# Kernel optimization log

Hardware: AMD Instinct MI355X
Metric: run time of the kernel (lower is better)

The kernel has to match this reference:

```python
import jax, jax.numpy as jnp
import numpy as np

N, F_IN, F_OUT, K = 4096, 32, 32, 2
NEG_SLOPE = 0.2
MASK_VAL = -9e15


def _sparse_mat(kv, km, density=0.01):
    vals = jax.random.normal(kv, (N, N), dtype=jnp.float32)
    mask = jax.random.uniform(km, (N, N)) < density
    return vals * mask


def setup_inputs() -> dict:
    key = jax.random.key(0)
    ks = jax.random.split(key, 12)
    x = jax.random.normal(ks[0], (N, F_IN), dtype=jnp.float32)
    Ld = _sparse_mat(ks[1], ks[2])
    Lu = _sparse_mat(ks[3], ks[4])
    P = jax.random.normal(ks[5], (N, N), dtype=jnp.float32) / np.sqrt(N)
    W1 = jax.random.normal(ks[6], (K, F_IN, F_OUT), dtype=jnp.float32) * 0.1
    W2 = jax.random.normal(ks[7], (K, F_IN, F_OUT), dtype=jnp.float32) * 0.1
    W0 = jax.random.normal(ks[8], (F_IN, F_OUT), dtype=jnp.float32) * 0.1
    att1 = jax.random.normal(ks[9], (2 * F_OUT * K, 1), dtype=jnp.float32) * 0.1
    att2 = jax.random.normal(ks[10], (2 * F_OUT * K, 1), dtype=jnp.float32) * 0.1
    return {"x": x, "Ld": Ld, "Lu": Lu, "P": P, "W1": W1, "W2": W2,
            "W0": W0, "att1": att1, "att2": att2}


def _branch(x, L, W, att):
    # W: [K, F_in, F_out]; precompute x @ W[k] for all k -> [K, N, F_out]
    Kk, _, Fo = W.shape
    xw = jnp.einsum('nf,kfo->kno', x, W)
    # torch.cat([x@W[k]], dim=1) == transpose+reshape of xw
    xcat = jnp.transpose(xw, (1, 0, 2)).reshape(x.shape[0], Kk * Fo)
    d = Fo * Kk
    e = xcat @ att[:d] + (xcat @ att[d:]).T            # [N, N]
    e = jax.nn.leaky_relu(e, negative_slope=NEG_SLOPE)
    e = jnp.where(L != 0, e, MASK_VAL)
    alpha = jax.nn.softmax(e, axis=1)                   # row softmax, no dropout (eval)
    z = alpha @ xw[0]
    a = alpha
    for k in range(1, Kk):
        a = a @ L
        z = z + a @ xw[k]
    return z


def reference(x, Ld, Lu, P, W1, W2, W0, att1, att2):
    z1 = _branch(x, Ld, W1, att1)
    z2 = _branch(x, Lu, W2, att2)
    x0 = P @ (x @ W0)
    return z1 + z2 + x0
```

## Files before the change

kernel.cpp:

```cpp
#include <hip/hip_runtime.h>
#include <hip/hip_bf16.h>

#define NN 4096
#define CAP 128
#define KS 8

typedef __attribute__((ext_vector_type(8))) short bf16x8;
typedef __attribute__((ext_vector_type(4))) float f32x4;

__device__ __forceinline__ float lrelu(float v) { return v >= 0.f ? v : 0.2f * v; }

__device__ __forceinline__ ushort f2bu(float f) {
    unsigned u = __float_as_uint(f);
    return (ushort)((u + 0x7FFFu + ((u >> 16) & 1u)) >> 16);
}

__global__ __launch_bounds__(256) void k_prep(
    const float* __restrict__ x,
    const float* __restrict__ W1, const float* __restrict__ W2,
    const float* __restrict__ W0,
    const float* __restrict__ att1, const float* __restrict__ att2,
    float* __restrict__ xwA1, float* __restrict__ xwB1,
    float* __restrict__ xwA2, float* __restrict__ xwB2,
    float* __restrict__ a1, float* __restrict__ b1,
    float* __restrict__ a2, float* __restrict__ b2,
    __hip_bfloat16* __restrict__ Bt)
{
    __shared__ float wl[5120];
    __shared__ float xs[256];
    const int t = threadIdx.x;
    for (int i = t; i < 2048; i += 256) { wl[i] = W1[i]; wl[2048 + i] = W2[i]; }
    for (int i = t; i < 1024; i += 256) wl[4096 + i] = W0[i];
    const int rowBase = blockIdx.x * 8;
    xs[t] = x[rowBase * 32 + t];
    __syncthreads();

    const int o = t & 31, r = t >> 5;
    const int row = rowBase + r;
    const float* xr = &xs[r * 32];
    float vA1 = 0.f, vB1 = 0.f, vA2 = 0.f, vB2 = 0.f, v0 = 0.f;
#pragma unroll
    for (int f = 0; f < 32; ++f) {
        const float xv = xr[f];
        vA1 += xv * wl[f * 32 + o];
        vB1 += xv * wl[1024 + f * 32 + o];
        vA2 += xv * wl[2048 + f * 32 + o];
        vB2 += xv * wl[3072 + f * 32 + o];
        v0  += xv * wl[4096 + f * 32 + o];
    }
    xwA1[row * 32 + o] = vA1;
    xwB1[row * 32 + o] = vB1;
    xwA2[row * 32 + o] = vA2;
    xwB2[row * 32 + o] = vB2;
    ((ushort*)Bt)[(size_t)o * NN + row] = f2bu(v0);

    float pa1 = vA1 * att1[o]      + vB1 * att1[32 + o];
    float pb1 = vA1 * att1[64 + o] + vB1 * att1[96 + o];
    float pa2 = vA2 * att2[o]      + vB2 * att2[32 + o];
    float pb2 = vA2 * att2[64 + o] + vB2 * att2[96 + o];
#pragma unroll
    for (int m = 1; m <= 16; m <<= 1) {
        pa1 += __shfl_xor(pa1, m); pb1 += __shfl_xor(pb1, m);
        pa2 += __shfl_xor(pa2, m); pb2 += __shfl_xor(pb2, m);
    }
    if (o == 0) { a1[row] = pa1; b1[row] = pb1; a2[row] = pa2; b2[row] = pb2; }
}

__global__ __launch_bounds__(256) void k_scan3(
    const float* __restrict__ Ld, const float* __restrict__ Lu,
    const float* __restrict__ xwB1, const float* __restrict__ xwB2,
    const float* __restrict__ xwA1, const float* __restrict__ xwA2,
    const float* __restrict__ a1, const float* __restrict__ b1,
    const float* __restrict__ a2, const float* __restrict__ b2,
    int2* __restrict__ csrv, int* __restrict__ cntArr,
    float* __restrict__ u1, float* __restrict__ u2)
{
    const int row = blockIdx.x;
    const int br  = blockIdx.y;
    const float* L   = br ? Lu : Ld;
    const float* xwB = br ? xwB2 : xwB1;
    const float* xwA = br ? xwA2 : xwA1;
    const float* aA  = br ? a2 : a1;
    const float* bA  = br ? b2 : b1;
    int2* csrB = csrv + ((size_t)br * NN + row) * CAP;
    float* u   = br ? u2 : u1;

    __shared__ int   sidx[CAP];
    __shared__ float sval[CAP];
    __shared__ int   wcnt[16];
    __shared__ float red[256];
    __shared__ float rpart[8];
    const int t = threadIdx.x;
    const int lane = t & 63, w = t >> 6;

    const float4* L4 = (const float4*)(L + (size_t)row * NN);
    float4 v[4];
#pragma unroll
    for (int it = 0; it < 4; ++it) v[it] = L4[it * 256 + t];

    const unsigned long long lt = (1ull << lane) - 1ull;

    int tots[4];
#pragma unroll
    for (int it = 0; it < 4; ++it) {
        const unsigned long long m0 = __ballot(v[it].x != 0.f);
        const unsigned long long m1 = __ballot(v[it].y != 0.f);
        const unsigned long long m2 = __ballot(v[it].z != 0.f);
        const unsigned long long m3 = __ballot(v[it].w != 0.f);
        tots[it] = __popcll(m0) + __popcll(m1) + __popcll(m2) + __popcll(m3);
    }
    if (lane == 0) {
        int4 tv; tv.x = tots[0]; tv.y = tots[1]; tv.z = tots[2]; tv.w = tots[3];
        *(int4*)&wcnt[w * 4] = tv;
    }
    __syncthreads();

    const int4 ca = *(const int4*)&wcnt[0];
    const int4 cb = *(const int4*)&wcnt[4];
    const int4 cc = *(const int4*)&wcnt[8];
    const int4 cd = *(const int4*)&wcnt[12];
    const int cs[16] = {ca.x, ca.y, ca.z, ca.w, cb.x, cb.y, cb.z, cb.w,
                        cc.x, cc.y, cc.z, cc.w, cd.x, cd.y, cd.z, cd.w};
    int total = 0;
#pragma unroll
    for (int k2 = 0; k2 < 16; ++k2) total += cs[k2];
    int base = 0;
#pragma unroll
    for (int k2 = 0; k2 < 16; ++k2) base += (k2 < (w << 2)) ? cs[k2] : 0;

    const int cnt  = min(total, CAP);
    const int cp16 = min((cnt + 15) & ~15, CAP);

#pragma unroll
    for (int it = 0; it < 4; ++it) {
        const float vx = v[it].x, vy = v[it].y, vz = v[it].z, vw = v[it].w;
        const unsigned long long m0 = __ballot(vx != 0.f);
        const unsigned long long m1 = __ballot(vy != 0.f);
        const unsigned long long m2 = __ballot(vz != 0.f);
        const unsigned long long m3 = __ballot(vw != 0.f);
        const int p0 = __popcll(m0), p1 = __popcll(m1), p2 = __popcll(m2);
        const int c0 = (it * 256 + t) * 4;
        int s;
        s = base + __popcll(m0 & lt);
        if (vx != 0.f && s < CAP) { sidx[s] = c0;     sval[s] = vx; }
        s = base + p0 + __popcll(m1 & lt);
        if (vy != 0.f && s < CAP) { sidx[s] = c0 + 1; sval[s] = vy; }
        s = base + p0 + p1 + __popcll(m2 & lt);
        if (vz != 0.f && s < CAP) { sidx[s] = c0 + 2; sval[s] = vz; }
        s = base + p0 + p1 + p2 + __popcll(m3 & lt);
        if (vw != 0.f && s < CAP) { sidx[s] = c0 + 3; sval[s] = vw; }
        base += p0 + p1 + p2 + __popcll(m3);
    }
    if (t >= cnt && t < cp16) { sidx[t] = 0; sval[t] = 0.f; }
    __syncthreads();

    const float ai = aA[row];
    const int myidx = (t < cp16) ? sidx[t] : 0;
    const float e = (t < cnt) ? lrelu(ai + bA[myidx]) : -1e30f;
    float m = e;
#pragma unroll
    for (int mm = 1; mm <= 32; mm <<= 1) m = fmaxf(m, __shfl_xor(m, mm));
    if (lane == 0) rpart[w] = m;
    __syncthreads();
    m = fmaxf(fmaxf(rpart[0], rpart[1]), fmaxf(rpart[2], rpart[3]));
    const float wgt = (t < cnt) ? __expf(e - m) : 0.f;
    float ss = wgt;
#pragma unroll
    for (int mm = 1; mm <= 32; mm <<= 1) ss += __shfl_xor(ss, mm);
    if (lane == 0) rpart[4 + w] = ss;
    __syncthreads();
    const float ssum = rpart[4] + rpart[5] + rpart[6] + rpart[7];
    const float inv = (cnt > 0) ? 1.f / ssum : 0.f;
    if (t < cp16) { int2 eo; eo.x = myidx; eo.y = __float_as_int(wgt * inv); csrB[t] = eo; }
    if (t == 0) cntArr[br * NN + row] = cnt;

    const int o = t & 31, g = t >> 5;
    float acc = 0.f;
    const int nPair = cp16 >> 4;
    if (nPair > 0) {
        float vA0 = sval[g],      vA1 = sval[g + 8];
        float xA0 = xwB[(size_t)sidx[g] * 32 + o];
        float xA1 = xwB[(size_t)sidx[g + 8] * 32 + o];
        for (int j = 1; j < nPair; ++j) {
            const int sB = g + 16 * j;
            const float vB0 = sval[sB],  vB1 = sval[sB + 8];
            const float xB0 = xwB[(size_t)sidx[sB] * 32 + o];
            const float xB1 = xwB[(size_t)sidx[sB + 8] * 32 + o];
            acc += vA0 * xA0 + vA1 * xA1;
            vA0 = vB0; xA0 = xB0; vA1 = vB1; xA1 = xB1;
        }
        acc += vA0 * xA0 + vA1 * xA1;
    }
    red[t] = acc;
    __syncthreads();
    if (t < 32) {
        float tot2 = 0.f;
#pragma unroll
        for (int g2 = 0; g2 < 8; ++g2) tot2 += red[g2 * 32 + t];
        u[(size_t)row * 32 + t] = tot2 + xwA[(size_t)row * 32 + t];
    }
}

__global__ __launch_bounds__(256) void k_accum(
    const int2* __restrict__ csrv, const int* __restrict__ cntArr,
    const float* __restrict__ u1, const float* __restrict__ u2,
    const float* __restrict__ partial, float* __restrict__ outp)
{
    __shared__ int2 sle[4][2 * CAP];
    const int w = threadIdx.x >> 6, lane = threadIdx.x & 63;
    const int row = blockIdx.x * 4 + w;
    const int o = lane & 31, g = lane >> 5;
    int2* se = sle[w];
    float total = 0.f;

    int cp[2];
#pragma unroll
    for (int br = 0; br < 2; ++br) {
        const int cnt = cntArr[br * NN + row];
        cp[br] = min((cnt + 15) & ~15, CAP);
        const int2* ci = csrv + ((size_t)br * NN + row) * CAP;
        if (lane < cp[br])      se[br * CAP + lane]      = ci[lane];
        if (lane + 64 < cp[br]) se[br * CAP + lane + 64] = ci[lane + 64];
    }

#pragma unroll
    for (int br = 0; br < 2; ++br) {
        const float* U = br ? u2 : u1;
        float acc = 0.f;
        const int nb = cp[br] >> 3;
        for (int j = 0; j < nb; ++j) {
            float wv[4], uv[4];
#pragma unroll
            for (int q = 0; q < 4; ++q) {
                const int2 e = se[br * CAP + 8 * j + 2 * q + g];
                wv[q] = __int_as_float(e.y);
                uv[q] = U[(size_t)e.x * 32 + o];
            }
#pragma unroll
            for (int q = 0; q < 4; ++q) acc += wv[q] * uv[q];
        }
        acc += __shfl_xor(acc, 32);
        total += acc;
    }

    if (lane < 32) {
#pragma unroll
        for (int p = 0; p < KS; ++p)
            total += partial[(size_t)p * NN * 32 + (size_t)row * 32 + o];
        outp[(size_t)row * 32 + o] = total;
    }
}

__global__ __launch_bounds__(256) void k_pgemm(
    const float* __restrict__ P, const ushort* __restrict__ Bt,
    float* __restrict__ partial)
{
    __shared__ ushort sA[2][16 * 64 * 8];
    __shared__ ushort sB[2][8 * 64 * 8];
    const int t = threadIdx.x;
    const int row0 = blockIdx.x * 64;
    const int ks = blockIdx.y;
    const float4*  P4  = (const float4*)P;
    const ushort4* Bt4 = (const ushort4*)Bt;

    const int lane = t & 63, w = t >> 6;

    f32x4 acc0 = {0.f, 0.f, 0.f, 0.f};
    f32x4 acc1 = {0.f, 0.f, 0.f, 0.f};

    auto stageA = [&](int c, int buf) {
        const int kc4 = (ks * 512 + c * 128) >> 2;
#pragma unroll
        for (int j = 0; j < 8; ++j) {
            const int i = t + 256 * j;
            const int row = i >> 5, q = i & 31;
            const float4 v = P4[(size_t)(row0 + row) * 1024 + kc4 + q];
            ushort4 u;
            u.x = f2bu(v.x); u.y = f2bu(v.y); u.z = f2bu(v.z); u.w = f2bu(v.w);
            const int wi = row >> 4, m = row & 15;
            const int kk = q >> 3, quad = (q >> 1) & 3, jj = q & 1;
            *(ushort4*)&sA[buf][(((wi * 4 + kk) * 64) + quad * 16 + m) * 8 + jj * 4] = u;
        }
    };
    auto stageB = [&](int c, int buf) {
        const int kc4 = (ks * 512 + c * 128) >> 2;
#pragma unroll
        for (int j = 0; j < 4; ++j) {
            const int i = t + 256 * j;
            const int o = i >> 5, q = i & 31;
            const ushort4 u = Bt4[(size_t)o * 1024 + kc4 + q];
            const int nt = o >> 4, n = o & 15;
            const int kk = q >> 3, quad = (q >> 1) & 3, jj = q & 1;
            *(ushort4*)&sB[buf][(((kk * 2 + nt) * 64) + quad * 16 + n) * 8 + jj * 4] = u;
        }
    };
    auto compute = [&](int buf) {
        const ushort* pa = &sA[buf][(w * 4) * 64 * 8 + lane * 8];
        const ushort* pb = &sB[buf][lane * 8];
#pragma unroll
        for (int kk = 0; kk < 4; ++kk) {
            const bf16x8 a  = *(const bf16x8*)(pa + kk * 512);
            const bf16x8 b0 = *(const bf16x8*)(pb + kk * 1024);
            const bf16x8 b1 = *(const bf16x8*)(pb + kk * 1024 + 512);
            acc0 = __builtin_amdgcn_mfma_f32_16x16x32_bf16(a, b0, acc0, 0, 0, 0);
            acc1 = __builtin_amdgcn_mfma_f32_16x16x32_bf16(a, b1, acc1, 0, 0, 0);
        }
    };

    stageA(0, 0); stageB(0, 0);
    __syncthreads();
    for (int c = 0; c < 4; ++c) {
        if (c < 3) { stageA(c + 1, (c + 1) & 1); stageB(c + 1, (c + 1) & 1); }
        compute(c & 1);
        __syncthreads();
    }

    const int m = lane & 15, quad = lane >> 4;
    float* out = partial + ((size_t)ks * NN + row0 + w * 16 + quad * 4) * 32;
#pragma unroll
    for (int r = 0; r < 4; ++r) {
        out[r * 32 + m]      = acc0[r];
        out[r * 32 + 16 + m] = acc1[r];
    }
}

extern "C" void kernel_launch(void* const* d_in, const int* in_sizes, int n_in,
                              void* d_out, int out_size, void* d_ws, size_t ws_size,
                              hipStream_t stream) {
    (void)in_sizes; (void)n_in; (void)out_size; (void)ws_size;
    const float* x    = (const float*)d_in[0];
    const float* Ld   = (const float*)d_in[1];
    const float* Lu   = (const float*)d_in[2];
    const float* P    = (const float*)d_in[3];
    const float* W1   = (const float*)d_in[4];
    const float* W2   = (const float*)d_in[5];
    const float* W0   = (const float*)d_in[6];
    const float* att1 = (const float*)d_in[7];
    const float* att2 = (const float*)d_in[8];

    float* ws = (float*)d_ws;
    float* xwA1 = ws;
    float* xwB1 = ws + 131072;
    float* xwA2 = ws + 262144;
    float* xwB2 = ws + 393216;
    float* u1   = ws + 524288;
    float* u2   = ws + 655360;
    float* a1   = ws + 786432;
    float* b1   = ws + 790528;
    float* a2   = ws + 794624;
    float* b2   = ws + 798720;
    float* partial = ws + 802816;
    __hip_bfloat16* Bt = (__hip_bfloat16*)(ws + 1851392);
    int2* csrv = (int2*)(ws + 1916928);
    int*  cnt  = (int*)(ws + 4014080);

    k_prep<<<512, 256, 0, stream>>>(x, W1, W2, W0, att1, att2,
                                    xwA1, xwB1, xwA2, xwB2, a1, b1, a2, b2, Bt);
    k_scan3<<<dim3(NN, 2), 256, 0, stream>>>(Ld, Lu, xwB1, xwB2, xwA1, xwA2,
                                             a1, b1, a2, b2, csrv, cnt, u1, u2);
    k_pgemm<<<dim3(64, KS), 256, 0, stream>>>(P, (const ushort*)Bt, partial);
    k_accum<<<NN / 4, 256, 0, stream>>>(csrv, cnt, u1, u2, partial,
                                        (float*)d_out);
}
```

Baseline: 223.5 us.

## Process one sparse row per wavefront in scan kernel, removing block syncs

The scan/compaction kernel now assigns one row per 64-lane wavefront (4 rows per block) instead of one row per 256-thread block. Each wave streams its row in four chunks with a running ballot prefix, keeps the compacted (index,value) list in per-wave LDS, and does the softmax and xwB gather with wave-level shuffles only. This removes the __syncthreads barriers and cross-wave reductions. In exchange each wave does four times as many serial loads per row, which may cut memory-level parallelism on this bandwidth-bound 128MB scan of Ld/Lu.

New measurement: 229.4 us. 2.6% more time.

```diff
diff --git a/kernel.cpp b/kernel.cpp
--- a/kernel.cpp
+++ b/kernel.cpp
@@ -66,7 +66,7 @@
     if (o == 0) { a1[row] = pa1; b1[row] = pb1; a2[row] = pa2; b2[row] = pb2; }
 }
 
-__global__ __launch_bounds__(256) void k_scan3(
+__global__ __launch_bounds__(256) void k_scan4(
     const float* __restrict__ Ld, const float* __restrict__ Lu,
     const float* __restrict__ xwB1, const float* __restrict__ xwB2,
     const float* __restrict__ xwA1, const float* __restrict__ xwA2,
@@ -75,7 +75,9 @@
     int2* __restrict__ csrv, int* __restrict__ cntArr,
     float* __restrict__ u1, float* __restrict__ u2)
 {
-    const int row = blockIdx.x;
+    const int t = threadIdx.x;
+    const int lane = t & 63, w = t >> 6;
+    const int row = blockIdx.x * 4 + w;
     const int br  = blockIdx.y;
     const float* L   = br ? Lu : Ld;
     const float* xwB = br ? xwB2 : xwB1;
@@ -85,120 +87,81 @@
     int2* csrB = csrv + ((size_t)br * NN + row) * CAP;
     float* u   = br ? u2 : u1;
 
-    __shared__ int   sidx[CAP];
-    __shared__ float sval[CAP];
-    __shared__ int   wcnt[16];
-    __shared__ float red[256];
-    __shared__ float rpart[8];
-    const int t = threadIdx.x;
-    const int lane = t & 63, w = t >> 6;
+    __shared__ int2 slist_all[4][CAP];
+    int2* slist = slist_all[w];
 
     const float4* L4 = (const float4*)(L + (size_t)row * NN);
-    float4 v[4];
-#pragma unroll
-    for (int it = 0; it < 4; ++it) v[it] = L4[it * 256 + t];
-
     const unsigned long long lt = (1ull << lane) - 1ull;
-
-    int tots[4];
-#pragma unroll
-    for (int it = 0; it < 4; ++it) {
-        const unsigned long long m0 = __ballot(v[it].x != 0.f);
-        const unsigned long long m1 = __ballot(v[it].y != 0.f);
-        const unsigned long long m2 = __ballot(v[it].z != 0.f);
-        const unsigned long long m3 = __ballot(v[it].w != 0.f);
-        tots[it] = __popcll(m0) + __popcll(m1) + __popcll(m2) + __popcll(m3);
-    }
-    if (lane == 0) {
-        int4 tv; tv.x = tots[0]; tv.y = tots[1]; tv.z = tots[2]; tv.w = tots[3];
-        *(int4*)&wcnt[w * 4] = tv;
-    }
-    __syncthreads();
-
-    const int4 ca = *(const int4*)&wcnt[0];
-    const int4 cb = *(const int4*)&wcnt[4];
-    const int4 cc = *(const int4*)&wcnt[8];
-    const int4 cd = *(const int4*)&wcnt[12];
-    const int cs[16] = {ca.x, ca.y, ca.z, ca.w, cb.x, cb.y, cb.z, cb.w,
-                        cc.x, cc.y, cc.z, cc.w, cd.x, cd.y, cd.z, cd.w};
-    int total = 0;
-#pragma unroll
-    for (int k2 = 0; k2 < 16; ++k2) total += cs[k2];
     int base = 0;
-#pragma unroll
-    for (int k2 = 0; k2 < 16; ++k2) base += (k2 < (w << 2)) ? cs[k2] : 0;
-
-    const int cnt  = min(total, CAP);
-    const int cp16 = min((cnt + 15) & ~15, CAP);
-
-#pragma unroll
-    for (int it = 0; it < 4; ++it) {
-        const float vx = v[it].x, vy = v[it].y, vz = v[it].z, vw = v[it].w;
-        const unsigned long long m0 = __ballot(vx != 0.f);
-        const unsigned long long m1 = __ballot(vy != 0.f);
-        const unsigned long long m2 = __ballot(vz != 0.f);
-        const unsigned long long m3 = __ballot(vw != 0.f);
-        const int p0 = __popcll(m0), p1 = __popcll(m1), p2 = __popcll(m2);
-        const int c0 = (it * 256 + t) * 4;
-        int s;
-        s = base + __popcll(m0 & lt);
-        if (vx != 0.f && s < CAP) { sidx[s] = c0;     sval[s] = vx; }
-        s = base + p0 + __popcll(m1 & lt);
-        if (vy != 0.f && s < CAP) { sidx[s] = c0 + 1; sval[s] = vy; }
-        s = base + p0 + p1 + __popcll(m2 & lt);
-        if (vz != 0.f && s < CAP) { sidx[s] = c0 + 2; sval[s] = vz; }
-        s = base + p0 + p1 + p2 + __popcll(m3 & lt);
-        if (vw != 0.f && s < CAP) { sidx[s] = c0 + 3; sval[s] = vw; }
-        base += p0 + p1 + p2 + __popcll(m3);
-    }
-    if (t >= cnt && t < cp16) { sidx[t] = 0; sval[t] = 0.f; }
-    __syncthreads();
+
+#pragma unroll 1
+    for (int c = 0; c < 4; ++c) {
+        float4 v[4];
+#pragma unroll
+        for (int j = 0; j < 4; ++j) v[j] = L4[c * 256 + j * 64 + lane];
+#pragma unroll
+        for (int j = 0; j < 4; ++j) {
+            const float vx = v[j].x, vy = v[j].y, vz = v[j].z, vw = v[j].w;
+            const unsigned long long m0 = __ballot(vx != 0.f);
+            const unsigned long long m1 = __ballot(vy != 0.f);
+            const unsigned long long m2 = __ballot(vz != 0.f);
+            const unsigned long long m3 = __ballot(vw != 0.f);
+            const int p0 = __popcll(m0), p1 = __popcll(m1), p2 = __popcll(m2);
+            const int c0 = (c * 256 + j * 64 + lane) * 4;
+            int s;
+            s = base + __popcll(m0 & lt);
+            if (vx != 0.f && s < CAP) { int2 e; e.x = c0;     e.y = __float_as_int(vx); slist[s] = e; }
+            s = base + p0 + __popcll(m1 & lt);
+            if (vy != 0.f && s < CAP) { int2 e; e.x = c0 + 1; e.y = __float_as_int(vy); slist[s] = e; }
+            s = base + p0 + p1 + __popcll(m2 & lt);
+            if (vz != 0.f && s < CAP) { int2 e; e.x = c0 + 2; e.y = __float_as_int(vz); slist[s] = e; }
+            s = base + p0 + p1 + p2 + __popcll(m3 & lt);
+            if (vw != 0.f && s < CAP) { int2 e; e.x = c0 + 3; e.y = __float_as_int(vw); slist[s] = e; }
+            base += p0 + p1 + p2 + __popcll(m3);
+        }
+    }
+
+    const int cnt  = min(base, CAP);
+    const int cpad = min((cnt + 15) & ~15, CAP);
+    const int ps = cnt + lane;
+    if (ps < cpad) { int2 z; z.x = 0; z.y = 0; slist[ps] = z; }
+
+    asm volatile("s_waitcnt lgkmcnt(0)" ::: "memory");
+    __builtin_amdgcn_sched_barrier(0);
 
     const float ai = aA[row];
-    const int myidx = (t < cp16) ? sidx[t] : 0;
-    const float e = (t < cnt) ? lrelu(ai + bA[myidx]) : -1e30f;
-    float m = e;
-#pragma unroll
-    for (int mm = 1; mm <= 32; mm <<= 1) m = fmaxf(m, __shfl_xor(m, mm));
-    if (lane == 0) rpart[w] = m;
-    __syncthreads();
-    m = fmaxf(fmaxf(rpart[0], rpart[1]), fmaxf(rpart[2], rpart[3]));
-    const float wgt = (t < cnt) ? __expf(e - m) : 0.f;
-    float ss = wgt;
+    int iA = 0, iB = 0;
+    float eA = -1e30f, eB = -1e30f;
+    if (lane < cnt)      { iA = slist[lane].x;      eA = lrelu(ai + bA[iA]); }
+    if (64 + lane < cnt) { iB = slist[64 + lane].x; eB = lrelu(ai + bA[iB]); }
+    float mx = fmaxf(eA, eB);
+#pragma unroll
+    for (int mm = 1; mm <= 32; mm <<= 1) mx = fmaxf(mx, __shfl_xor(mx, mm));
+    const float w0 = (lane < cnt)      ? __expf(eA - mx) : 0.f;
+    const float w1 = (64 + lane < cnt) ? __expf(eB - mx) : 0.f;
+    float ss = w0 + w1;
 #pragma unroll
     for (int mm = 1; mm <= 32; mm <<= 1) ss += __shfl_xor(ss, mm);
-    if (lane == 0) rpart[4 + w] = ss;
-    __syncthreads();
-    const float ssum = rpart[4] + rpart[5] + rpart[6] + rpart[7];
-    const float inv = (cnt > 0) ? 1.f / ssum : 0.f;
-    if (t < cp16) { int2 eo; eo.x = myidx; eo.y = __float_as_int(wgt * inv); csrB[t] = eo; }
-    if (t == 0) cntArr[br * NN + row] = cnt;
-
-    const int o = t & 31, g = t >> 5;
+    const float inv = (cnt > 0) ? 1.f / ss : 0.f;
+    if (lane < cpad)      { int2 eo; eo.x = iA; eo.y = __float_as_int(w0 * inv); csrB[lane] = eo; }
+    if (64 + lane < cpad) { int2 eo; eo.x = iB; eo.y = __float_as_int(w1 * inv); csrB[64 + lane] = eo; }
+    if (lane == 0) cntArr[br * NN + row] = cnt;
+
+    const int o = lane & 31, g = lane >> 5;
     float acc = 0.f;
-    const int nPair = cp16 >> 4;
-    if (nPair > 0) {
-        float vA0 = sval[g],      vA1 = sval[g + 8];
-        float xA0 = xwB[(size_t)sidx[g] * 32 + o];
-        float xA1 = xwB[(size_t)sidx[g + 8] * 32 + o];
-        for (int j = 1; j < nPair; ++j) {
-            const int sB = g + 16 * j;
-            const float vB0 = sval[sB],  vB1 = sval[sB + 8];
-            const float xB0 = xwB[(size_t)sidx[sB] * 32 + o];
-            const float xB1 = xwB[(size_t)sidx[sB + 8] * 32 + o];
-            acc += vA0 * xA0 + vA1 * xA1;
-            vA0 = vB0; xA0 = xB0; vA1 = vB1; xA1 = xB1;
-        }
-        acc += vA0 * xA0 + vA1 * xA1;
-    }
-    red[t] = acc;
-    __syncthreads();
-    if (t < 32) {
-        float tot2 = 0.f;
-#pragma unroll
-        for (int g2 = 0; g2 < 8; ++g2) tot2 += red[g2 * 32 + t];
-        u[(size_t)row * 32 + t] = tot2 + xwA[(size_t)row * 32 + t];
-    }
+    for (int s0 = 0; s0 < cpad; s0 += 8) {
+        float vv[4], uu[4];
+#pragma unroll
+        for (int q = 0; q < 4; ++q) {
+            const int2 e = slist[s0 + 2 * q + g];
+            vv[q] = __int_as_float(e.y);
+            uu[q] = xwB[(size_t)e.x * 32 + o];
+        }
+#pragma unroll
+        for (int q = 0; q < 4; ++q) acc += vv[q] * uu[q];
+    }
+    acc += __shfl_xor(acc, 32);
+    if (lane < 32) u[(size_t)row * 32 + o] = acc + xwA[(size_t)row * 32 + o];
 }
 
 __global__ __launch_bounds__(256) void k_accum(
@@ -356,8 +319,8 @@
 
     k_prep<<<512, 256, 0, stream>>>(x, W1, W2, W0, att1, att2,
                                     xwA1, xwB1, xwA2, xwB2, a1, b1, a2, b2, Bt);
-    k_scan3<<<dim3(NN, 2), 256, 0, stream>>>(Ld, Lu, xwB1, xwB2, xwA1, xwA2,
-                                             a1, b1, a2, b2, csrv, cnt, u1, u2);
+    k_scan4<<<dim3(NN / 4, 2), 256, 0, stream>>>(Ld, Lu, xwB1, xwB2, xwA1, xwA2,
+                                                 a1, b1, a2, b2, csrv, cnt, u1, u2);
     k_pgemm<<<dim3(64, KS), 256, 0, stream>>>(P, (const ushort*)Bt, partial);
     k_accum<<<NN / 4, 256, 0, stream>>>(csrv, cnt, u1, u2, partial,
                                         (float*)d_out);
```

## Split scan per branch, reuse ballot masks, and drop LDS staging in P-GEMM

Applied to the files above, without the earlier changes.

The two-branch scan kernel becomes one kernel launched once per branch, with branch-specific pointers passed as arguments instead of being selected from blockIdx.y. The ballot masks from the counting pass are kept in registers, so the scatter pass no longer recomputes them. The P·(xW0) GEMM loses its shared-memory double-buffered staging: each wave now loads P rows and Bt directly from global memory, converts them to bf16 in registers and feeds the MFMAs. This removes LDS traffic and barriers, but adds an extra launch and gives up coalesced, shared-memory tiled loads.

Result: slower. 231.1 us (+3.4%).

```diff
diff --git a/kernel.cpp b/kernel.cpp
--- a/kernel.cpp
+++ b/kernel.cpp
@@ -66,24 +66,15 @@
     if (o == 0) { a1[row] = pa1; b1[row] = pb1; a2[row] = pa2; b2[row] = pb2; }
 }
 
-__global__ __launch_bounds__(256) void k_scan3(
-    const float* __restrict__ Ld, const float* __restrict__ Lu,
-    const float* __restrict__ xwB1, const float* __restrict__ xwB2,
-    const float* __restrict__ xwA1, const float* __restrict__ xwA2,
-    const float* __restrict__ a1, const float* __restrict__ b1,
-    const float* __restrict__ a2, const float* __restrict__ b2,
+__global__ __launch_bounds__(256) void k_scan6(
+    const float* __restrict__ L,
+    const float* __restrict__ xwB, const float* __restrict__ xwA,
+    const float* __restrict__ aA, const float* __restrict__ bA,
     int2* __restrict__ csrv, int* __restrict__ cntArr,
-    float* __restrict__ u1, float* __restrict__ u2)
+    float* __restrict__ u)
 {
     const int row = blockIdx.x;
-    const int br  = blockIdx.y;
-    const float* L   = br ? Lu : Ld;
-    const float* xwB = br ? xwB2 : xwB1;
-    const float* xwA = br ? xwA2 : xwA1;
-    const float* aA  = br ? a2 : a1;
-    const float* bA  = br ? b2 : b1;
-    int2* csrB = csrv + ((size_t)br * NN + row) * CAP;
-    float* u   = br ? u2 : u1;
+    int2* csrB = csrv + (size_t)row * CAP;
 
     __shared__ int   sidx[CAP];
     __shared__ float sval[CAP];
@@ -100,14 +91,15 @@
 
     const unsigned long long lt = (1ull << lane) - 1ull;
 
+    unsigned long long M0[4], M1[4], M2[4], M3[4];
     int tots[4];
 #pragma unroll
     for (int it = 0; it < 4; ++it) {
-        const unsigned long long m0 = __ballot(v[it].x != 0.f);
-        const unsigned long long m1 = __ballot(v[it].y != 0.f);
-        const unsigned long long m2 = __ballot(v[it].z != 0.f);
-        const unsigned long long m3 = __ballot(v[it].w != 0.f);
-        tots[it] = __popcll(m0) + __popcll(m1) + __popcll(m2) + __popcll(m3);
+        M0[it] = __ballot(v[it].x != 0.f);
+        M1[it] = __ballot(v[it].y != 0.f);
+        M2[it] = __ballot(v[it].z != 0.f);
+        M3[it] = __ballot(v[it].w != 0.f);
+        tots[it] = __popcll(M0[it]) + __popcll(M1[it]) + __popcll(M2[it]) + __popcll(M3[it]);
     }
     if (lane == 0) {
         int4 tv; tv.x = tots[0]; tv.y = tots[1]; tv.z = tots[2]; tv.w = tots[3];
@@ -134,22 +126,18 @@
 #pragma unroll
     for (int it = 0; it < 4; ++it) {
         const float vx = v[it].x, vy = v[it].y, vz = v[it].z, vw = v[it].w;
-        const unsigned long long m0 = __ballot(vx != 0.f);
-        const unsigned long long m1 = __ballot(vy != 0.f);
-        const unsigned long long m2 = __ballot(vz != 0.f);
-        const unsigned long long m3 = __ballot(vw != 0.f);
-        const int p0 = __popcll(m0), p1 = __popcll(m1), p2 = __popcll(m2);
+        const int p0 = __popcll(M0[it]), p1 = __popcll(M1[it]), p2 = __popcll(M2[it]);
         const int c0 = (it * 256 + t) * 4;
         int s;
-        s = base + __popcll(m0 & lt);
+        s = base + __popcll(M0[it] & lt);
         if (vx != 0.f && s < CAP) { sidx[s] = c0;     sval[s] = vx; }
-        s = base + p0 + __popcll(m1 & lt);
+        s = base + p0 + __popcll(M1[it] & lt);
         if (vy != 0.f && s < CAP) { sidx[s] = c0 + 1; sval[s] = vy; }
-        s = base + p0 + p1 + __popcll(m2 & lt);
+        s = base + p0 + p1 + __popcll(M2[it] & lt);
         if (vz != 0.f && s < CAP) { sidx[s] = c0 + 2; sval[s] = vz; }
-        s = base + p0 + p1 + p2 + __popcll(m3 & lt);
+        s = base + p0 + p1 + p2 + __popcll(M3[it] & lt);
         if (vw != 0.f && s < CAP) { sidx[s] = c0 + 3; sval[s] = vw; }
-        base += p0 + p1 + p2 + __popcll(m3);
+        base += p0 + p1 + p2 + __popcll(M3[it]);
     }
     if (t >= cnt && t < cp16) { sidx[t] = 0; sval[t] = 0.f; }
     __syncthreads();
@@ -172,7 +160,7 @@
     const float ssum = rpart[4] + rpart[5] + rpart[6] + rpart[7];
     const float inv = (cnt > 0) ? 1.f / ssum : 0.f;
     if (t < cp16) { int2 eo; eo.x = myidx; eo.y = __float_as_int(wgt * inv); csrB[t] = eo; }
-    if (t == 0) cntArr[br * NN + row] = cnt;
+    if (t == 0) cntArr[row] = cnt;
 
     const int o = t & 31, g = t >> 5;
     float acc = 0.f;
@@ -251,76 +239,46 @@
     }
 }
 
-__global__ __launch_bounds__(256) void k_pgemm(
+__global__ __launch_bounds__(256) void k_pgemm2(
     const float* __restrict__ P, const ushort* __restrict__ Bt,
     float* __restrict__ partial)
 {
-    __shared__ ushort sA[2][16 * 64 * 8];
-    __shared__ ushort sB[2][8 * 64 * 8];
     const int t = threadIdx.x;
-    const int row0 = blockIdx.x * 64;
-    const int ks = blockIdx.y;
-    const float4*  P4  = (const float4*)P;
-    const ushort4* Bt4 = (const ushort4*)Bt;
-
     const int lane = t & 63, w = t >> 6;
+    const int gw = blockIdx.x * 4 + w;
+    const int mt = gw & 255;
+    const int ks = gw >> 8;
+    const int m0 = mt * 16;
+    const int r  = lane & 15;
+    const int kq = lane >> 4;
+
+    const float*  pa  = P  + (size_t)(m0 + r) * NN + ks * 512 + kq * 8;
+    const ushort* pb0 = Bt + (size_t)r        * NN + ks * 512 + kq * 8;
+    const ushort* pb1 = Bt + (size_t)(16 + r) * NN + ks * 512 + kq * 8;
 
     f32x4 acc0 = {0.f, 0.f, 0.f, 0.f};
     f32x4 acc1 = {0.f, 0.f, 0.f, 0.f};
 
-    auto stageA = [&](int c, int buf) {
-        const int kc4 = (ks * 512 + c * 128) >> 2;
-#pragma unroll
-        for (int j = 0; j < 8; ++j) {
-            const int i = t + 256 * j;
-            const int row = i >> 5, q = i & 31;
-            const float4 v = P4[(size_t)(row0 + row) * 1024 + kc4 + q];
-            ushort4 u;
-            u.x = f2bu(v.x); u.y = f2bu(v.y); u.z = f2bu(v.z); u.w = f2bu(v.w);
-            const int wi = row >> 4, m = row & 15;
-            const int kk = q >> 3, quad = (q >> 1) & 3, jj = q & 1;
-            *(ushort4*)&sA[buf][(((wi * 4 + kk) * 64) + quad * 16 + m) * 8 + jj * 4] = u;
-        }
-    };
-    auto stageB = [&](int c, int buf) {
-        const int kc4 = (ks * 512 + c * 128) >> 2;
-#pragma unroll
-        for (int j = 0; j < 4; ++j) {
-            const int i = t + 256 * j;
-            const int o = i >> 5, q = i & 31;
-            const ushort4 u = Bt4[(size_t)o * 1024 + kc4 + q];
-            const int nt = o >> 4, n = o & 15;
-            const int kk = q >> 3, quad = (q >> 1) & 3, jj = q & 1;
-            *(ushort4*)&sB[buf][(((kk * 2 + nt) * 64) + quad * 16 + n) * 8 + jj * 4] = u;
-        }
-    };
-    auto compute = [&](int buf) {
-        const ushort* pa = &sA[buf][(w * 4) * 64 * 8 + lane * 8];
-        const ushort* pb = &sB[buf][lane * 8];
-#pragma unroll
-        for (int kk = 0; kk < 4; ++kk) {
-            const bf16x8 a  = *(const bf16x8*)(pa + kk * 512);
-            const bf16x8 b0 = *(const bf16x8*)(pb + kk * 1024);
-            const bf16x8 b1 = *(const bf16x8*)(pb + kk * 1024 + 512);
-            acc0 = __builtin_amdgcn_mfma_f32_16x16x32_bf16(a, b0, acc0, 0, 0, 0);
-            acc1 = __builtin_amdgcn_mfma_f32_16x16x32_bf16(a, b1, acc1, 0, 0, 0);
-        }
-    };
-
-    stageA(0, 0); stageB(0, 0);
-    __syncthreads();
-    for (int c = 0; c < 4; ++c) {
-        if (c < 3) { stageA(c + 1, (c + 1) & 1); stageB(c + 1, (c + 1) & 1); }
-        compute(c & 1);
-        __syncthreads();
-    }
-
-    const int m = lane & 15, quad = lane >> 4;
-    float* out = partial + ((size_t)ks * NN + row0 + w * 16 + quad * 4) * 32;
-#pragma unroll
-    for (int r = 0; r < 4; ++r) {
-        out[r * 32 + m]      = acc0[r];
-        out[r * 32 + 16 + m] = acc1[r];
+#pragma unroll 4
+    for (int kk = 0; kk < 16; ++kk) {
+        const float4 a0 = *(const float4*)(pa + kk * 32);
+        const float4 a1 = *(const float4*)(pa + kk * 32 + 4);
+        const bf16x8 b0 = *(const bf16x8*)(pb0 + kk * 32);
+        const bf16x8 b1 = *(const bf16x8*)(pb1 + kk * 32);
+        bf16x8 a;
+        a[0] = (short)f2bu(a0.x); a[1] = (short)f2bu(a0.y);
+        a[2] = (short)f2bu(a0.z); a[3] = (short)f2bu(a0.w);
+        a[4] = (short)f2bu(a1.x); a[5] = (short)f2bu(a1.y);
+        a[6] = (short)f2bu(a1.z); a[7] = (short)f2bu(a1.w);
+        acc0 = __builtin_amdgcn_mfma_f32_16x16x32_bf16(a, b0, acc0, 0, 0, 0);
+        acc1 = __builtin_amdgcn_mfma_f32_16x16x32_bf16(a, b1, acc1, 0, 0, 0);
+    }
+
+    float* out = partial + ((size_t)ks * NN + m0 + kq * 4) * 32;
+#pragma unroll
+    for (int rr = 0; rr < 4; ++rr) {
+        out[rr * 32 + r]      = acc0[rr];
+        out[rr * 32 + 16 + r] = acc1[rr];
     }
 }
 
@@ -356,9 +314,11 @@
 
     k_prep<<<512, 256, 0, stream>>>(x, W1, W2, W0, att1, att2,
                                     xwA1, xwB1, xwA2, xwB2, a1, b1, a2, b2, Bt);
-    k_scan3<<<dim3(NN, 2), 256, 0, stream>>>(Ld, Lu, xwB1, xwB2, xwA1, xwA2,
-                                             a1, b1, a2, b2, csrv, cnt, u1, u2);
-    k_pgemm<<<dim3(64, KS), 256, 0, stream>>>(P, (const ushort*)Bt, partial);
+    k_scan6<<<NN, 256, 0, stream>>>(Ld, xwB1, xwA1, a1, b1,
+                                    csrv, cnt, u1);
+    k_scan6<<<NN, 256, 0, stream>>>(Lu, xwB2, xwA2, a2, b2,
+                                    csrv + (size_t)NN * CAP, cnt + NN, u2);
+    k_pgemm2<<<512, 256, 0, stream>>>(P, (const ushort*)Bt, partial);
     k_accum<<<NN / 4, 256, 0, stream>>>(csrv, cnt, u1, u2, partial,
                                         (float*)d_out);
 }
```
